# Optimization experiments

Measured on AMD Instinct MI355X. Metric: run time of the kernel, lower is better.

## Reference

```python
import jax, jax.numpy as jnp
import numpy as np

N_FEATURES = 32
HIDDEN_DIM = 64
B, T = 512, 1024


def lstm(x, w_ih, w_hh, b_ih, b_hh):
    """PyTorch-compatible single-layer LSTM, batch_first.
    x: [B, T, F_in]; w_ih: [4H, F_in]; w_hh: [4H, H]; b_ih, b_hh: [4H].
    Gate order (PyTorch): i, f, g, o. Returns outputs [B, T, H].
    """
    Bq, Tq, _ = x.shape
    H = w_hh.shape[1]
    # Precompute input contribution for all timesteps (big GEMM, time-parallel)
    x_gates = jnp.einsum('btf,gf->btg', x, w_ih) + b_ih + b_hh  # [B, T, 4H]
    x_gates = jnp.swapaxes(x_gates, 0, 1)  # [T, B, 4H]

    def step(carry, xg):
        h, c = carry
        gates = xg + h @ w_hh.T  # [B, 4H]
        i = jax.nn.sigmoid(gates[:, 0 * H:1 * H])
        f = jax.nn.sigmoid(gates[:, 1 * H:2 * H])
        g = jnp.tanh(gates[:, 2 * H:3 * H])
        o = jax.nn.sigmoid(gates[:, 3 * H:4 * H])
        c = f * c + i * g
        h = o * jnp.tanh(c)
        return (h, c), h

    h0 = jnp.zeros((Bq, H), dtype=x.dtype)
    c0 = jnp.zeros((Bq, H), dtype=x.dtype)
    _, hs = jax.lax.scan(step, (h0, c0), x_gates)  # hs: [T, B, H]
    return jnp.swapaxes(hs, 0, 1)  # [B, T, H]


def setup_inputs() -> dict:
    key = jax.random.key(0)
    ks = jax.random.split(key, 9)
    F, H = N_FEATURES, HIDDEN_DIM
    s_enc = 1.0 / np.sqrt(H)
    s_dec = 1.0 / np.sqrt(F)
    return {
        'x': jax.random.normal(ks[0], (B, T, F), dtype=jnp.float32),
        # encoder: input F -> hidden H
        'enc_w_ih': jax.random.uniform(ks[1], (4 * H, F), jnp.float32, -s_enc, s_enc),
        'enc_w_hh': jax.random.uniform(ks[2], (4 * H, H), jnp.float32, -s_enc, s_enc),
        'enc_b_ih': jax.random.uniform(ks[3], (4 * H,), jnp.float32, -s_enc, s_enc),
        'enc_b_hh': jax.random.uniform(ks[4], (4 * H,), jnp.float32, -s_enc, s_enc),
        # decoder: input H -> hidden F
        'dec_w_ih': jax.random.uniform(ks[5], (4 * F, H), jnp.float32, -s_dec, s_dec),
        'dec_w_hh': jax.random.uniform(ks[6], (4 * F, F), jnp.float32, -s_dec, s_dec),
        'dec_b_ih': jax.random.uniform(ks[7], (4 * F,), jnp.float32, -s_dec, s_dec),
        'dec_b_hh': jax.random.uniform(ks[8], (4 * F,), jnp.float32, -s_dec, s_dec),
    }


def reference(x, enc_w_ih, enc_w_hh, enc_b_ih, enc_b_hh,
              dec_w_ih, dec_w_hh, dec_b_ih, dec_b_hh):
    encoded = lstm(x, enc_w_ih, enc_w_hh, enc_b_ih, enc_b_hh)      # [B, T, H]
    decoded = lstm(encoded, dec_w_ih, dec_w_hh, dec_b_ih, dec_b_hh)  # [B, T, F]
    return decoded
```

## Files before the change

### kernel.cpp

```cpp
#include <hip/hip_runtime.h>
#include <stdint.h>
#include <math.h>

#define TT 1024
#define FF 32
#define HH 64

typedef unsigned int u32;
typedef _Float16 f16;
typedef __attribute__((ext_vector_type(8))) _Float16 half8;
typedef __attribute__((ext_vector_type(4))) float v4f;

#define L2E  1.44269504088896341f
#define L2E2 2.88539008177792681f

__device__ __forceinline__ float fsig_s(float s) {
    return __builtin_amdgcn_rcpf(1.f + __builtin_amdgcn_exp2f(-s));
}
__device__ __forceinline__ float ftanh_s(float s) {
    return 2.f * __builtin_amdgcn_rcpf(1.f + __builtin_amdgcn_exp2f(-s)) - 1.f;
}

__device__ __forceinline__ half8 ld8h(const float* p, float sc) {
    float4 a = *(const float4*)p, b = *(const float4*)(p + 4);
    half8 r;
    r[0] = (f16)(a.x * sc); r[1] = (f16)(a.y * sc); r[2] = (f16)(a.z * sc); r[3] = (f16)(a.w * sc);
    r[4] = (f16)(b.x * sc); r[5] = (f16)(b.y * sc); r[6] = (f16)(b.z * sc); r[7] = (f16)(b.w * sc);
    return r;
}


__global__ __launch_bounds__(256, 2)
void lstm_ae_mfma(const float* __restrict__ x,
                  const float* __restrict__ ewih, const float* __restrict__ ewhh,
                  const float* __restrict__ ebih, const float* __restrict__ ebhh,
                  const float* __restrict__ dwih, const float* __restrict__ dwhh,
                  const float* __restrict__ dbih, const float* __restrict__ dbhh,
                  float* __restrict__ out)
{
    const int b = blockIdx.x;
    const int t = threadIdx.x;
    const int w = t >> 6;
    const int l = t & 63;
    const int q = l >> 4;
    const int n = l & 15;

    __shared__ __align__(16) f16 Bst[2][2][160];
    __shared__ __align__(16) float xst[2][2048];

    const float sc = ((n & 3) == 2) ? L2E2 : L2E;
    half8 af[6][3];
#pragma unroll
    for (int i = 0; i < 6; ++i) {
        int tile = w * 6 + i;
        if (tile < 16) {
            int r = (n & 3) * 64 + tile * 4 + (n >> 2);
            af[i][0] = ld8h(ewhh + r * 64 + q * 8, sc);
            af[i][1] = ld8h(ewhh + r * 64 + 32 + q * 8, sc);
            af[i][2] = ld8h(ewih + r * 32 + q * 8, sc);
        } else {
            int r = (n & 3) * 32 + (tile - 16) * 4 + (n >> 2);
            af[i][0] = ld8h(dwih + r * 64 + q * 8, sc);
            af[i][1] = ld8h(dwih + r * 64 + 32 + q * 8, sc);
            af[i][2] = ld8h(dwhh + r * 32 + q * 8, sc);
        }
    }

    const int sel = n >> 1;
    const bool act = (n < 12);
    const int tile_s = w * 6 + (sel < 6 ? sel : 0);
    const bool is_enc = (tile_s < 16);
    const int u = is_enc ? (tile_s * 4 + q) : ((tile_s - 16) * 4 + q);

    float b0 = 0.f, b1 = 0.f, b2 = 0.f, b3 = 0.f, c_st = 0.f;
    if (act) {
        if (is_enc) {
            b0 = ebih[u]       + ebhh[u];
            b1 = ebih[64 + u]  + ebhh[64 + u];
            b2 = ebih[128 + u] + ebhh[128 + u];
            b3 = ebih[192 + u] + ebhh[192 + u];
        } else {
            b0 = dbih[u]      + dbhh[u];
            b1 = dbih[32 + u] + dbhh[32 + u];
            b2 = dbih[64 + u] + dbhh[64 + u];
            b3 = dbih[96 + u] + dbhh[96 + u];
        }
    }
    b0 *= L2E; b1 *= L2E; b2 *= L2E2; b3 *= L2E;

    { u32* bz = (u32*)&Bst[0][0][0]; for (int i2 = t; i2 < 2 * 2 * 160 / 2; i2 += 256) bz[i2] = 0u; }
    const float* xb = x + (size_t)b * TT * FF;
    *(float4*)&xst[0][t * 8]     = *(const float4*)(xb + t * 8);
    *(float4*)&xst[0][t * 8 + 4] = *(const float4*)(xb + t * 8 + 4);
    __syncthreads();
    if (t >= 96 && t < 128) Bst[0][0][64 + (t - 96)] = (f16)xst[0][t - 96];
    __syncthreads();

    for (int tt = 0; tt <= TT; ++tt) {
        const int p = tt & 1;

        float4 px0, px1;
        const int cn = (tt >> 6) + 1;
        const bool pf = ((tt & 63) == 0) && (cn < 16);
        if (pf) {
            px0 = *(const float4*)(xb + cn * 2048 + t * 8);
            px1 = *(const float4*)(xb + cn * 2048 + t * 8 + 4);
        }

        const f16* Bp = &Bst[p][0][0];
        const int cb = (n & 1) * 160 + q * 8;
        half8 bf0 = *(const half8*)(Bp + cb);
        half8 bf1 = *(const half8*)(Bp + cb + 32);
        half8 bf2 = *(const half8*)(Bp + cb + 64);
        half8 bf3 = *(const half8*)(Bp + cb + 96);

        v4f zero = {0.f, 0.f, 0.f, 0.f};
        v4f acc[6];
#pragma unroll
        for (int i = 0; i < 6; ++i)
            acc[i] = __builtin_amdgcn_mfma_f32_16x16x32_f16(af[i][0], bf0, zero, 0, 0, 0);
#pragma unroll
        for (int i = 0; i < 6; ++i)
            acc[i] = __builtin_amdgcn_mfma_f32_16x16x32_f16(af[i][1], bf1, acc[i], 0, 0, 0);
#pragma unroll
        for (int i = 0; i < 6; ++i)
            acc[i] = __builtin_amdgcn_mfma_f32_16x16x32_f16(af[i][2], (w * 6 + i < 16) ? bf2 : bf3,
                                                            acc[i], 0, 0, 0);

        v4f u_ = acc[0];
#pragma unroll
        for (int i = 1; i < 6; ++i) if (sel == i) u_ = acc[i];

        v4f s_;
#pragma unroll
        for (int e = 0; e < 4; ++e) {
            int tmp = __builtin_amdgcn_update_dpp(0, __float_as_int(u_[e]), 0xB1, 0xF, 0xF, true);
            s_[e] = u_[e] + __int_as_float(tmp);
        }

        f16* Bw = &Bst[p ^ 1][0][0];
        if (act && (is_enc ? (tt < TT) : (tt >= 1))) {
            float i_ = fsig_s(s_[0] + b0);
            float f_ = fsig_s(s_[1] + b1);
            float g_ = ftanh_s(s_[2] + b2);
            float o_ = fsig_s(s_[3] + b3);
            c_st = f_ * c_st + L2E2 * (i_ * g_);
            float h = o_ * ftanh_s(c_st);
            f16 hi = (f16)h;
            f16 lo = (f16)(h - (float)hi);
            const int kk = is_enc ? u : (96 + u);
            Bw[(n & 1) * 160 + kk] = (n & 1) ? lo : hi;
            if (!is_enc && !(n & 1))
                out[(size_t)b * TT * FF + (size_t)(tt - 1) * FF + u] = h;
        } else if (n == 12 || n == 13) {
            int st = tt + 1;
            if (st < TT) {
                int j = w * 8 + q * 2 + (n - 12);
                Bw[64 + j] = (f16)xst[(st >> 6) & 1][(st & 63) * 32 + j];
            }
        }

        if (pf) {
            *(float4*)&xst[cn & 1][t * 8]     = px0;
            *(float4*)&xst[cn & 1][t * 8 + 4] = px1;
        }

        asm volatile("s_waitcnt lgkmcnt(0)" ::: "memory");
        __builtin_amdgcn_s_barrier();
        __builtin_amdgcn_sched_barrier(0);
    }
}

extern "C" void kernel_launch(void* const* d_in, const int* in_sizes, int n_in,
                              void* d_out, int out_size, void* d_ws, size_t ws_size,
                              hipStream_t stream) {
    (void)in_sizes; (void)n_in; (void)out_size; (void)d_ws; (void)ws_size;
    lstm_ae_mfma<<<512, 256, 0, stream>>>((const float*)d_in[0],
                                          (const float*)d_in[1], (const float*)d_in[2],
                                          (const float*)d_in[3], (const float*)d_in[4],
                                          (const float*)d_in[5], (const float*)d_in[6],
                                          (const float*)d_in[7], (const float*)d_in[8],
                                          (float*)d_out);
}
```

Measured before the change: 731.3 us.

## Precompute next-step encoder input MFMA off the recurrent critical path

The encoder's input-projection MFMA for step t+1 is now issued during step t and used as the accumulator seed for the next step's recurrent MFMAs. This shortens the dependent MFMA chain per timestep. x is kept in shared memory as fp16 and read directly as the B operand, so the per-step copy of x into the state buffer goes away and the state buffer shrinks. It also adds a uniform wave index via readfirstlane and an s_sleep stagger for half the blocks, which only shifts when those blocks start.

```diff
diff --git a/kernel.cpp b/kernel.cpp
--- a/kernel.cpp
+++ b/kernel.cpp
@@ -5,6 +5,7 @@
 #define TT 1024
 #define FF 32
 #define HH 64
+#define CST 112
 
 typedef unsigned int u32;
 typedef _Float16 f16;
@@ -41,12 +42,14 @@
     const int b = blockIdx.x;
     const int t = threadIdx.x;
     const int w = t >> 6;
+    const int wu = __builtin_amdgcn_readfirstlane(w);
     const int l = t & 63;
     const int q = l >> 4;
     const int n = l & 15;
 
-    __shared__ __align__(16) f16 Bst[2][2][160];
-    __shared__ __align__(16) float xst[2][2048];
+    __shared__ __align__(16) f16 Bst[2][2][CST];
+    __shared__ __align__(16) f16 xh16[2][64][32];
+    __shared__ __align__(16) f16 zp[8];
 
     const float sc = ((n & 3) == 2) ? L2E2 : L2E;
     half8 af[6][3];
@@ -71,6 +74,7 @@
     const int tile_s = w * 6 + (sel < 6 ? sel : 0);
     const bool is_enc = (tile_s < 16);
     const int u = is_enc ? (tile_s * 4 + q) : ((tile_s - 16) * 4 + q);
+    const int wk1 = (n & 1) * CST + (is_enc ? u : 64 + u);
 
     float b0 = 0.f, b1 = 0.f, b2 = 0.f, b3 = 0.f, c_st = 0.f;
     if (act) {
@@ -88,13 +92,34 @@
     }
     b0 *= L2E; b1 *= L2E; b2 *= L2E2; b3 *= L2E;
 
-    { u32* bz = (u32*)&Bst[0][0][0]; for (int i2 = t; i2 < 2 * 2 * 160 / 2; i2 += 256) bz[i2] = 0u; }
+    { u32* bz = (u32*)&Bst[0][0][0]; if (t < 2 * 2 * CST / 2) bz[t] = 0u; }
+    if (t < 4) ((u32*)zp)[t] = 0u;
     const float* xb = x + (size_t)b * TT * FF;
-    *(float4*)&xst[0][t * 8]     = *(const float4*)(xb + t * 8);
-    *(float4*)&xst[0][t * 8 + 4] = *(const float4*)(xb + t * 8 + 4);
+    {
+        float4 a0 = *(const float4*)(xb + t * 8);
+        float4 a1 = *(const float4*)(xb + t * 8 + 4);
+        half8 hx;
+        hx[0] = (f16)a0.x; hx[1] = (f16)a0.y; hx[2] = (f16)a0.z; hx[3] = (f16)a0.w;
+        hx[4] = (f16)a1.x; hx[5] = (f16)a1.y; hx[6] = (f16)a1.z; hx[7] = (f16)a1.w;
+        *(half8*)&xh16[0][t >> 2][(t & 3) * 8] = hx;
+    }
     __syncthreads();
-    if (t >= 96 && t < 128) Bst[0][0][64 + (t - 96)] = (f16)xst[0][t - 96];
-    __syncthreads();
+
+    v4f zero = {0.f, 0.f, 0.f, 0.f};
+
+    v4f accx[6];
+#pragma unroll
+    for (int i = 0; i < 6; ++i) accx[i] = zero;
+    {
+        const f16* xpn = (n & 1) ? zp : &xh16[0][0][q * 8];
+        half8 bx0 = *(const half8*)xpn;
+#pragma unroll
+        for (int i = 0; i < 6; ++i)
+            if (wu * 6 + i < 16)
+                accx[i] = __builtin_amdgcn_mfma_f32_16x16x32_f16(af[i][2], bx0, zero, 0, 0, 0);
+    }
+
+    if ((b >> 8) & 1) asm volatile("s_sleep 6");
 
     for (int tt = 0; tt <= TT; ++tt) {
         const int p = tt & 1;
@@ -108,24 +133,26 @@
         }
 
         const f16* Bp = &Bst[p][0][0];
-        const int cb = (n & 1) * 160 + q * 8;
+        const int cb = (n & 1) * CST + q * 8;
         half8 bf0 = *(const half8*)(Bp + cb);
         half8 bf1 = *(const half8*)(Bp + cb + 32);
-        half8 bf2 = *(const half8*)(Bp + cb + 64);
-        half8 bf3 = *(const half8*)(Bp + cb + 96);
-
-        v4f zero = {0.f, 0.f, 0.f, 0.f};
+        half8 bf3 = *(const half8*)(Bp + cb + 64);
+        const int sx = tt + 1;
+        const f16* xpn = (n & 1) ? zp : &xh16[(sx >> 6) & 1][sx & 63][q * 8];
+        half8 bx = *(const half8*)xpn;
+
         v4f acc[6];
 #pragma unroll
-        for (int i = 0; i < 6; ++i)
-            acc[i] = __builtin_amdgcn_mfma_f32_16x16x32_f16(af[i][0], bf0, zero, 0, 0, 0);
-#pragma unroll
-        for (int i = 0; i < 6; ++i)
-            acc[i] = __builtin_amdgcn_mfma_f32_16x16x32_f16(af[i][1], bf1, acc[i], 0, 0, 0);
-#pragma unroll
-        for (int i = 0; i < 6; ++i)
-            acc[i] = __builtin_amdgcn_mfma_f32_16x16x32_f16(af[i][2], (w * 6 + i < 16) ? bf2 : bf3,
-                                                            acc[i], 0, 0, 0);
+        for (int i = 0; i < 6; ++i) {
+            v4f s1 = __builtin_amdgcn_mfma_f32_16x16x32_f16(af[i][0], bf0, accx[i], 0, 0, 0);
+            v4f s2 = __builtin_amdgcn_mfma_f32_16x16x32_f16(af[i][1], bf1, s1, 0, 0, 0);
+            if (wu * 6 + i < 16) {
+                acc[i] = s2;
+                accx[i] = __builtin_amdgcn_mfma_f32_16x16x32_f16(af[i][2], bx, zero, 0, 0, 0);
+            } else {
+                acc[i] = __builtin_amdgcn_mfma_f32_16x16x32_f16(af[i][2], bf3, s2, 0, 0, 0);
+            }
+        }
 
         v4f u_ = acc[0];
 #pragma unroll
@@ -148,21 +175,16 @@
             float h = o_ * ftanh_s(c_st);
             f16 hi = (f16)h;
             f16 lo = (f16)(h - (float)hi);
-            const int kk = is_enc ? u : (96 + u);
-            Bw[(n & 1) * 160 + kk] = (n & 1) ? lo : hi;
+            Bw[wk1] = (n & 1) ? lo : hi;
             if (!is_enc && !(n & 1))
                 out[(size_t)b * TT * FF + (size_t)(tt - 1) * FF + u] = h;
-        } else if (n == 12 || n == 13) {
-            int st = tt + 1;
-            if (st < TT) {
-                int j = w * 8 + q * 2 + (n - 12);
-                Bw[64 + j] = (f16)xst[(st >> 6) & 1][(st & 63) * 32 + j];
-            }
         }
 
         if (pf) {
-            *(float4*)&xst[cn & 1][t * 8]     = px0;
-            *(float4*)&xst[cn & 1][t * 8 + 4] = px1;
+            half8 hx;
+            hx[0] = (f16)px0.x; hx[1] = (f16)px0.y; hx[2] = (f16)px0.z; hx[3] = (f16)px0.w;
+            hx[4] = (f16)px1.x; hx[5] = (f16)px1.y; hx[6] = (f16)px1.z; hx[7] = (f16)px1.w;
+            *(half8*)&xh16[cn & 1][t >> 2][(t & 3) * 8] = hx;
         }
 
         asm volatile("s_waitcnt lgkmcnt(0)" ::: "memory");
```

Measured after the change: 773.4 us. +5.8%, slower.
